# Kernel tuning notes

Hardware: AMD Instinct MI355X
Metric: run time of the kernel (lower is better)

Reference implementation:

```python
import jax, jax.numpy as jnp
import numpy as np

B, C_IN, FH, FW = 4, 256, 64, 176
N_PTS = 150000
D_BINS = 64
BEV_H = BEV_W = 200
RES = 0.5
EPS = 1e-5


def setup_inputs() -> dict:
    key = jax.random.key(0)
    ks = jax.random.split(key, 8)
    camera_features = jax.random.normal(ks[0], (B, C_IN, FH, FW), dtype=jnp.float32)
    pixels_uv = jax.random.uniform(ks[1], (B, N_PTS, 2), dtype=jnp.float32)
    K_inv = jax.random.normal(ks[2], (B, 3, 3), dtype=jnp.float32)
    # depth head params: Conv2d(256,128,3,pad=1) -> BN(128) -> ReLU -> Conv2d(128,64,1)
    W1 = jax.random.normal(ks[3], (128, C_IN, 3, 3), dtype=jnp.float32) * 0.02
    b1 = jnp.zeros((128,), dtype=jnp.float32)
    gamma = jnp.ones((128,), dtype=jnp.float32)
    beta = jnp.zeros((128,), dtype=jnp.float32)
    W2 = jax.random.normal(ks[4], (D_BINS, 128, 1, 1), dtype=jnp.float32) * 0.05
    b2 = jnp.zeros((D_BINS,), dtype=jnp.float32)
    depth_bins = jnp.linspace(1.0, 60.0, D_BINS, dtype=jnp.float32)
    return {"camera_features": camera_features, "pixels_uv": pixels_uv, "K_inv": K_inv,
            "W1": W1, "b1": b1, "gamma": gamma, "beta": beta, "W2": W2, "b2": b2,
            "depth_bins": depth_bins}


def _depth_head(x, W1, b1, gamma, beta, W2, b2):
    dn = ("NCHW", "OIHW", "NCHW")
    h = jax.lax.conv_general_dilated(x, W1, (1, 1), ((1, 1), (1, 1)), dimension_numbers=dn)
    h = h + b1[None, :, None, None]
    # BatchNorm2d, training-mode batch statistics (module is used without eval())
    mu = h.mean(axis=(0, 2, 3), keepdims=True)
    var = h.var(axis=(0, 2, 3), keepdims=True)
    h = (h - mu) * jax.lax.rsqrt(var + EPS)
    h = h * gamma[None, :, None, None] + beta[None, :, None, None]
    h = jax.nn.relu(h)
    logits = jax.lax.conv_general_dilated(h, W2, (1, 1), ((0, 0), (0, 0)), dimension_numbers=dn)
    logits = logits + b2[None, :, None, None]
    return jax.nn.softmax(logits, axis=1)  # [B, D, H, W]


def reference(camera_features, pixels_uv, K_inv, W1, b1, gamma, beta, W2, b2, depth_bins):
    depth_dist = _depth_head(camera_features, W1, b1, gamma, beta, W2, b2)

    # lift_to_3d
    exp_d = depth_dist.mean(axis=1)  # [B, H, W]
    ones = jnp.ones((B, N_PTS, 1), dtype=pixels_uv.dtype)
    homo = jnp.concatenate([pixels_uv, ones], axis=-1)            # [B, N, 3]
    pts3d = jnp.einsum('bnk,bjk->bnj', homo, K_inv)               # homo @ K_inv^T
    depth = exp_d.mean(axis=(1, 2))[:, None, None]                # [B, 1, 1]
    pts3d = pts3d * depth                                         # [B, N, 3]

    # splat_to_bev: scatter-add occupancy, then clamp to [0, 1]
    x_min = -(BEV_H * RES / 2)
    gx = jnp.clip(((pts3d[:, :, 0] - x_min) / RES).astype(jnp.int32), 0, BEV_W - 1)
    gy = jnp.clip(((pts3d[:, :, 1] - x_min) / RES).astype(jnp.int32), 0, BEV_H - 1)
    flat_idx = (jnp.arange(B, dtype=jnp.int32)[:, None] * (BEV_H * BEV_W) + gy * BEV_W + gx).ravel()
    grid = jnp.zeros((B * BEV_H * BEV_W,), dtype=jnp.float32).at[flat_idx].add(1.0)
    bev_grid = jnp.clip(grid.reshape(B, BEV_H, BEV_W), 0.0, 1.0)

    # expected_depth
    exp_depth = (depth_dist * depth_bins[None, :, None, None]).sum(axis=1)  # [B, H, W]

    return bev_grid, depth_dist, exp_depth, pts3d
```

## Files before the change

### kernel.cpp

```cpp
#include <hip/hip_runtime.h>

#define BATCH 4
#define CIN 256
#define FH 64
#define FW 176
#define HW (FH*FW)
#define PHW 11748
#define C1 128
#define DBINS 64
#define NPTS 150000
#define BEVN 200
#define EPSV 1e-5f

#define OFF_BEV 0
#define OFF_DD  160000
#define OFF_ED  3043584
#define OFF_PTS 3088640

#define WSB_H    0
#define WSB_WT   11534336
#define WSB_W2B  12124160
#define WSB_BN   12140544
#define WSB_XTP  12144640
#define XTP_B_ELEMS 3007488
#define WS_NEED_FULL  36204544ull
#define WS_NEED_HALF  24174592ull

typedef short bfx8 __attribute__((ext_vector_type(8)));
typedef short bfx4 __attribute__((ext_vector_type(4)));
typedef float f32x4 __attribute__((ext_vector_type(4)));
typedef unsigned short u16;

__device__ __forceinline__ u16 f2bf(float f) {
  union { float f; unsigned int u; } v; v.f = f;
  unsigned int r = v.u + 0x7FFF + ((v.u >> 16) & 1);
  return (u16)(r >> 16);
}
__device__ __forceinline__ float bf2f(u16 h) {
  union { unsigned int u; float f; } v; v.u = ((unsigned int)h) << 16;
  return v.f;
}

__device__ __forceinline__ void gload_lds16(const void* g, void* l) {
  __builtin_amdgcn_global_load_lds(
      (const __attribute__((address_space(1))) unsigned int*)g,
      (__attribute__((address_space(3))) unsigned int*)l, 16, 0, 0);
}

__global__ __launch_bounds__(256) void k_init(
    float* __restrict__ out, u16* __restrict__ w2b,
    const float* __restrict__ W2, u16* __restrict__ wt,
    const float* __restrict__ W1, u16* __restrict__ xtp, int nb) {
  int idx = blockIdx.x * 256 + threadIdx.x;
  if (idx < BATCH * BEVN * BEVN) out[OFF_BEV + idx] = 0.0f;
  if (idx < DBINS * C1) w2b[idx] = f2bf(W2[idx]);
  if (idx < 9 * C1 * CIN) {
    int tap = idx >> 15, rem = idx & 32767;
    int co = rem >> 8, c = rem & 255;
    wt[idx] = f2bf(W1[(co * CIN + c) * 9 + tap]);
  }
  const int nbord = nb * 484 * 32;
  if (idx < nbord) {
    int bloc = idx / (484 * 32);
    int r = idx - bloc * 484 * 32;
    int bpx = r >> 5, ch8 = r & 31;
    int prow, pcol;
    if (bpx < 178)      { prow = 0;  pcol = bpx; }
    else if (bpx < 356) { prow = 65; pcol = bpx - 178; }
    else { int q = bpx - 356; prow = 1 + (q >> 1); pcol = (q & 1) * 177; }
    *(bfx8*)&xtp[(bloc * PHW + prow * 178 + pcol) * 256 + ch8 * 8] = (bfx8)(short)0;
  }
}

__global__ __launch_bounds__(256) void k_xt(
    const float* __restrict__ x, u16* __restrict__ xtp, int b0) {
  __shared__ u16 s_t[176 * 72];
  const int blk = blockIdx.x;
  const int bloc = blk >> 8;
  const int rem = blk & 255;
  const int row = rem >> 2;
  const int c0 = (rem & 3) * 64;
  const int b = b0 + bloc;
  const int t = threadIdx.x;
  #pragma unroll
  for (int i = 0; i < 44; ++i) {
    int f = i * 256 + t;
    int c = f / 176, px = f - c * 176;
    s_t[px * 72 + c] = f2bf(x[((b * CIN + c0 + c) * FH + row) * FW + px]);
  }
  __syncthreads();
  const int base = (bloc * PHW + (row + 1) * 178 + 1) * 256 + c0;
  #pragma unroll
  for (int i = 0; i < 6; ++i) {
    int f = i * 256 + t;
    if (f < 1408) {
      int px = f >> 3, s = f & 7;
      *(bfx8*)&xtp[base + (px << 8) + s * 8] = *(const bfx8*)&s_t[px * 72 + s * 8];
    }
  }
}

#define ABUF_E 2048
#define STEP_E 6144

__global__ __launch_bounds__(256) void k_conv(
    const u16* __restrict__ xTp, const u16* __restrict__ wt,
    const float* __restrict__ b1, u16* __restrict__ hbf, int b0) {
  __shared__ __align__(16) u16 sMem[3 * STEP_E];

  const int blk = blockIdx.x;
  const int bloc = blk / 176;
  const int tile = blk % 176;
  const int h0 = (tile / 11) * 4;
  const int w0 = (tile % 11) * 16;
  const int b = b0 + bloc;
  const int t = threadIdx.x;
  const int lane = t & 63;
  const int wv = t >> 6;
  const int mw = wv >> 1, nw = wv & 1;
  const int l15 = lane & 15, kg = lane >> 4;

  const int cA = wv * 64 + lane;
  {
  }
  const int pxA = cA >> 2;
  const int gA = (bloc * PHW + (h0 + (pxA >> 4)) * 178 + (w0 + (pxA & 15))) * 256
               + (((cA & 3) ^ ((cA >> 3) & 3)) << 3);
  int gB[2];
  #pragma unroll
  for (int j = 0; j < 2; ++j) {
    int c = cA + j * 256;
    gB[j] = (c >> 2) * 256 + (((c & 3) ^ ((c >> 3) & 3)) << 3);
  }
  const int sw8 = (kg ^ ((l15 >> 1) & 3)) << 3;

  f32x4 acc[2][4];
  #pragma unroll
  for (int mf = 0; mf < 2; ++mf)
    #pragma unroll
    for (int nf = 0; nf < 4; ++nf) acc[mf][nf] = (f32x4)(0.f);

#define STAGE(S, SEL)                                                          \
  {                                                                            \
    const int tap_ = (S) >> 3, ck_ = (S) & 7;                                  \
    const int dy_ = tap_ / 3, dx_ = tap_ - dy_ * 3;                            \
    const int ao_ = ((dy_ * 178 + dx_) << 8) + (ck_ << 5);                     \
    const int wo_ = tap_ * 32768 + (ck_ << 5);                                 \
    u16* lb_ = &sMem[(SEL) * STEP_E];                                          \
    gload_lds16(&xTp[gA + ao_], &lb_[(wv * 64) * 8]);                          \
    gload_lds16(&wt[gB[0] + wo_], &lb_[ABUF_E + (wv * 64) * 8]);               \
    gload_lds16(&wt[gB[1] + wo_], &lb_[ABUF_E + (wv * 64 + 256) * 8]);         \
  }

#define COMPUTE(SEL)                                                           \
  {                                                                            \
    const u16* lb_ = &sMem[(SEL) * STEP_E];                                    \
    bfx8 af[2], bf[4];                                                         \
    _Pragma("unroll")                                                          \
    for (int mf = 0; mf < 2; ++mf)                                             \
      af[mf] = *(const bfx8*)&lb_[(mw * 32 + mf * 16 + l15) * 32 + sw8];       \
    _Pragma("unroll")                                                          \
    for (int nf = 0; nf < 4; ++nf)                                             \
      bf[nf] = *(const bfx8*)&lb_[ABUF_E + (nw * 64 + nf * 16 + l15) * 32 + sw8]; \
    _Pragma("unroll")                                                          \
    for (int mf = 0; mf < 2; ++mf)                                             \
      _Pragma("unroll")                                                        \
      for (int nf = 0; nf < 4; ++nf)                                           \
        acc[mf][nf] = __builtin_amdgcn_mfma_f32_16x16x32_bf16(af[mf], bf[nf], acc[mf][nf], 0, 0, 0); \
  }

#define VMCNT(N) asm volatile("s_waitcnt vmcnt(" #N ")" ::: "memory")
#define BARR __builtin_amdgcn_s_barrier()
#define SCHED0 __builtin_amdgcn_sched_barrier(0)

  STAGE(0, 0);
  STAGE(1, 1);
  STAGE(2, 2);

  #pragma unroll 1
  for (int s = 0; s <= 66; s += 3) {
    VMCNT(6); BARR; SCHED0;
    COMPUTE(0);
    BARR;
    STAGE(s + 3, 0);
    VMCNT(6); BARR; SCHED0;
    COMPUTE(1);
    BARR;
    STAGE(s + 4, 1);
    VMCNT(6); BARR; SCHED0;
    COMPUTE(2);
    BARR;
    STAGE(s + 5, 2);
  }
  VMCNT(6); BARR; SCHED0;
  COMPUTE(0);
  VMCNT(3); BARR; SCHED0;
  COMPUTE(1);
  VMCNT(0); BARR; SCHED0;
  COMPUTE(2);

  #pragma unroll
  for (int mf = 0; mf < 2; ++mf) {
    const int py = h0 + mw * 2 + mf;
    #pragma unroll
    for (int nf = 0; nf < 4; ++nf) {
      const int co = nw * 64 + nf * 16 + l15;
      const float bb = b1[co];
      bfx4 hv;
      #pragma unroll
      for (int j = 0; j < 4; ++j) hv[j] = (short)f2bf(acc[mf][nf][j] + bb);
      *(bfx4*)&hbf[((b * C1 + co) * FH + py) * FW + w0 + kg * 4] = hv;
    }
  }
#undef STAGE
#undef COMPUTE
#undef VMCNT
#undef BARR
#undef SCHED0
}

__global__ __launch_bounds__(256) void k_bnsum(
    const u16* __restrict__ h, float* __restrict__ part) {
  const int ch = blockIdx.x >> 2, b = blockIdx.x & 3;
  const int t = threadIdx.x;
  float s = 0.f, q = 0.f;
  const bfx8* p = (const bfx8*)&h[(b * C1 + ch) * HW];
  for (int i = t; i < HW / 8; i += 256) {
    bfx8 v8 = p[i];
    #pragma unroll
    for (int j = 0; j < 8; ++j) {
      float v = bf2f((u16)v8[j]);
      s += v;
      q = fmaf(v, v, q);
    }
  }
  #pragma unroll
  for (int o = 32; o; o >>= 1) {
    s += __shfl_xor(s, o);
    q += __shfl_xor(q, o);
  }
  __shared__ float rs[4], rq[4];
  int w = t >> 6;
  if ((t & 63) == 0) { rs[w] = s; rq[w] = q; }
  __syncthreads();
  if (t == 0) {
    part[ch * 8 + b * 2 + 0] = rs[0] + rs[1] + rs[2] + rs[3];
    part[ch * 8 + b * 2 + 1] = rq[0] + rq[1] + rq[2] + rq[3];
  }
}

__global__ __launch_bounds__(256) void k_head(
    const u16* __restrict__ h, const float* __restrict__ part,
    const float* __restrict__ gamma, const float* __restrict__ beta,
    const u16* __restrict__ w2b, const float* __restrict__ b2,
    const float* __restrict__ bins, float* __restrict__ out) {
  __shared__ u16 sAct[64 * 128];
  __shared__ float sP[64 * 68];
  __shared__ float sAB[256];

  const int blk = blockIdx.x;
  const int b = blk / 176;
  const int px0 = (blk % 176) * 64;
  const int t = threadIdx.x;
  const int lane = t & 63;
  const int w = t >> 6;
  const int l15 = lane & 15, kg = lane >> 4;

  if (t < 128) {
    float s = 0.f, q = 0.f;
    #pragma unroll
    for (int bb = 0; bb < 4; ++bb) {
      s += part[t * 8 + bb * 2 + 0];
      q += part[t * 8 + bb * 2 + 1];
    }
    const float inv_n = 1.0f / (float)(BATCH * HW);
    float mu = s * inv_n;
    float var = q * inv_n - mu * mu;
    float a = gamma[t] * rsqrtf(var + EPSV);
    sAB[t] = a;
    sAB[128 + t] = beta[t] - mu * a;
  }

  bfx8 bfr[4][4];
  #pragma unroll
  for (int nf = 0; nf < 4; ++nf)
    #pragma unroll
    for (int ck = 0; ck < 4; ++ck)
      bfr[nf][ck] = *(const bfx8*)&w2b[(nf * 16 + l15) * 128 + ck * 32 + kg * 8];
  float binr[4], b2r[4];
  #pragma unroll
  for (int nf = 0; nf < 4; ++nf) {
    binr[nf] = bins[nf * 16 + l15];
    b2r[nf] = b2[nf * 16 + l15];
  }
  f32x4 acc[4];
  #pragma unroll
  for (int nf = 0; nf < 4; ++nf) acc[nf] = (f32x4)(b2r[nf]);
  __syncthreads();

  #pragma unroll
  for (int i = 0; i < 4; ++i) {
    int f = t + i * 256;
    int c = f >> 3, g = f & 7;
    bfx8 v8 = *(const bfx8*)&h[(b * C1 + c) * HW + px0 + g * 8];
    float a = sAB[c], sh = sAB[128 + c];
    #pragma unroll
    for (int j = 0; j < 8; ++j) {
      int px = g * 8 + j;
      float v = fmaxf(fmaf(bf2f((u16)v8[j]), a, sh), 0.f);
      sAct[px * 128 + (((c >> 3) ^ (px & 15)) << 3) + (c & 7)] = f2bf(v);
    }
  }
  __syncthreads();

  #pragma unroll
  for (int ck = 0; ck < 4; ++ck) {
    bfx8 af = *(const bfx8*)&sAct[(w * 16 + l15) * 128 + (((ck * 4 + kg) ^ l15) << 3)];
    #pragma unroll
    for (int nf = 0; nf < 4; ++nf)
      acc[nf] = __builtin_amdgcn_mfma_f32_16x16x32_bf16(af, bfr[nf][ck], acc[nf], 0, 0, 0);
  }

  #pragma unroll
  for (int j = 0; j < 4; ++j) {
    float e[4];
    float z = 0.f, ez = 0.f;
    #pragma unroll
    for (int nf = 0; nf < 4; ++nf) {
      e[nf] = __expf(acc[nf][j]);
      z += e[nf];
      ez = fmaf(e[nf], binr[nf], ez);
    }
    #pragma unroll
    for (int o = 1; o < 16; o <<= 1) {
      z += __shfl_xor(z, o);
      ez += __shfl_xor(ez, o);
    }
    float inv = 1.0f / z;
    int px = w * 16 + kg * 4 + j;
    #pragma unroll
    for (int nf = 0; nf < 4; ++nf)
      sP[(nf * 16 + l15) * 68 + px] = e[nf] * inv;
    if (l15 == kg * 4 + j) out[OFF_ED + b * HW + px0 + px] = ez * inv;
  }
  __syncthreads();

  #pragma unroll
  for (int i = 0; i < 4; ++i) {
    int f = t + i * 256;
    int d = f >> 4, q = f & 15;
    f32x4 v;
    #pragma unroll
    for (int jj = 0; jj < 4; ++jj) v[jj] = sP[d * 68 + q * 4 + jj];
    *(f32x4*)&out[OFF_DD + (b * DBINS + d) * HW + px0 + q * 4] = v;
  }
}

__global__ void k_points(const float* __restrict__ uv, const float* __restrict__ kinv,
                         float* __restrict__ out) {
  int idx = blockIdx.x * 256 + threadIdx.x;
  if (idx >= BATCH * NPTS) return;
  int b = idx / NPTS;
  const float depth = 1.0f / 64.0f;
  float u = uv[idx * 2 + 0];
  float v = uv[idx * 2 + 1];
  const float* K = &kinv[b * 9];
  float p0 = (u * K[0] + v * K[1] + K[2]) * depth;
  float p1 = (u * K[3] + v * K[4] + K[5]) * depth;
  float p2 = (u * K[6] + v * K[7] + K[8]) * depth;
  out[OFF_PTS + idx * 3 + 0] = p0;
  out[OFF_PTS + idx * 3 + 1] = p1;
  out[OFF_PTS + idx * 3 + 2] = p2;
  int gx = (int)((p0 + 50.0f) * 2.0f);
  int gy = (int)((p1 + 50.0f) * 2.0f);
  gx = min(max(gx, 0), BEVN - 1);
  gy = min(max(gy, 0), BEVN - 1);
  out[OFF_BEV + (b * BEVN + gy) * BEVN + gx] = 1.0f;
}

extern "C" void kernel_launch(void* const* d_in, const int* in_sizes, int n_in,
                              void* d_out, int out_size, void* d_ws, size_t ws_size,
                              hipStream_t stream) {
  const float* x     = (const float*)d_in[0];
  const float* uv    = (const float*)d_in[1];
  const float* kinv  = (const float*)d_in[2];
  const float* w1    = (const float*)d_in[3];
  const float* b1    = (const float*)d_in[4];
  const float* gamma = (const float*)d_in[5];
  const float* beta  = (const float*)d_in[6];
  const float* w2    = (const float*)d_in[7];
  const float* b2    = (const float*)d_in[8];
  const float* bins  = (const float*)d_in[9];
  float* out = (float*)d_out;

  u16*   wsH   = (u16*)d_ws;
  u16*   wsWT  = (u16*)((char*)d_ws + WSB_WT);
  u16*   wsW2B = (u16*)((char*)d_ws + WSB_W2B);
  float* wsBN  = (float*)((char*)d_ws + WSB_BN);
  u16*   wsXTP = (u16*)((char*)d_ws + WSB_XTP);

  int nb = (ws_size >= WS_NEED_FULL) ? 4 : (ws_size >= WS_NEED_HALF) ? 2 : 1;

  k_init<<<1152, 256, 0, stream>>>(out, wsW2B, w2, wsWT, w1, wsXTP, nb);
  for (int b0 = 0; b0 < BATCH; b0 += nb) {
    k_xt<<<nb * 256, 256, 0, stream>>>(x, wsXTP, b0);
    k_conv<<<nb * 176, 256, 0, stream>>>(wsXTP, wsWT, b1, wsH, b0);
  }
  k_bnsum<<<512, 256, 0, stream>>>(wsH, wsBN);
  k_head<<<704, 256, 0, stream>>>(wsH, wsBN, gamma, beta, wsW2B, b2, bins, out);
  k_points<<<(BATCH * NPTS + 255) / 256, 256, 0, stream>>>(uv, kinv, out);
}
```

Before: 87.66 us.

## Restructure conv as halo-tile implicit GEMM with register-held weights

The 3x3 conv kernel now stages an 8x18 input halo tile per 32-channel chunk in LDS and reuses it across all 9 taps. Before, each tap reloaded its own shifted input slice. Weights are read straight from global memory into registers, and the tile now covers 8 rows by 64 output channels. Both halves of the output channels are split across blocks, and a double-buffered halo replaces the triple-buffered per-tap staging. The aim is to cut global/LDS traffic and barriers per MFMA, at the cost of uncoalesced direct weight loads and more register pressure (launch bounds 256,2).

```diff
diff --git a/kernel.cpp b/kernel.cpp
--- a/kernel.cpp
+++ b/kernel.cpp
@@ -100,18 +100,19 @@
   }
 }
 
-#define ABUF_E 2048
-#define STEP_E 6144
-
-__global__ __launch_bounds__(256) void k_conv(
+#define HALO_E 6144
+
+__global__ __launch_bounds__(256, 2) void k_conv(
     const u16* __restrict__ xTp, const u16* __restrict__ wt,
     const float* __restrict__ b1, u16* __restrict__ hbf, int b0) {
-  __shared__ __align__(16) u16 sMem[3 * STEP_E];
+  __shared__ __align__(16) u16 sMem[2 * HALO_E];
 
   const int blk = blockIdx.x;
   const int bloc = blk / 176;
-  const int tile = blk % 176;
-  const int h0 = (tile / 11) * 4;
+  const int rem = blk % 176;
+  const int co0 = (rem & 1) * 64;
+  const int tile = rem >> 1;
+  const int h0 = (tile / 11) * 8;
   const int w0 = (tile % 11) * 16;
   const int b = b0 + bloc;
   const int t = threadIdx.x;
@@ -120,91 +121,85 @@
   const int mw = wv >> 1, nw = wv & 1;
   const int l15 = lane & 15, kg = lane >> 4;
 
-  const int cA = wv * 64 + lane;
-  {
-  }
-  const int pxA = cA >> 2;
-  const int gA = (bloc * PHW + (h0 + (pxA >> 4)) * 178 + (w0 + (pxA & 15))) * 256
-               + (((cA & 3) ^ ((cA >> 3) & 3)) << 3);
-  int gB[2];
-  #pragma unroll
-  for (int j = 0; j < 2; ++j) {
-    int c = cA + j * 256;
-    gB[j] = (c >> 2) * 256 + (((c & 3) ^ ((c >> 3) & 3)) << 3);
-  }
-  const int sw8 = (kg ^ ((l15 >> 1) & 3)) << 3;
-
-  f32x4 acc[2][4];
-  #pragma unroll
-  for (int mf = 0; mf < 2; ++mf)
-    #pragma unroll
-    for (int nf = 0; nf < 4; ++nf) acc[mf][nf] = (f32x4)(0.f);
-
-#define STAGE(S, SEL)                                                          \
+  int gH[3];
+  #pragma unroll
+  for (int j = 0; j < 3; ++j) {
+    int c = t + j * 256;
+    int px = c >> 2;
+    if (px > 179) px = 179;
+    int hr = px / 18, hc = px - hr * 18;
+    int slog = (c & 3) ^ ((c >> 3) & 3);
+    gH[j] = (bloc * PHW + (h0 + hr) * 178 + (w0 + hc)) * 256 + slog * 8;
+  }
+  const int gwB0 = (co0 + nw * 32 + l15) * 256 + kg * 8;
+  const int gwB1 = (co0 + nw * 32 + 16 + l15) * 256 + kg * 8;
+
+  f32x4 acc[4][2];
+  #pragma unroll
+  for (int mf = 0; mf < 4; ++mf)
+    #pragma unroll
+    for (int nf = 0; nf < 2; ++nf) acc[mf][nf] = (f32x4)(0.f);
+
+#define STAGEH(CKV, DST)                                                       \
   {                                                                            \
-    const int tap_ = (S) >> 3, ck_ = (S) & 7;                                  \
-    const int dy_ = tap_ / 3, dx_ = tap_ - dy_ * 3;                            \
-    const int ao_ = ((dy_ * 178 + dx_) << 8) + (ck_ << 5);                     \
-    const int wo_ = tap_ * 32768 + (ck_ << 5);                                 \
-    u16* lb_ = &sMem[(SEL) * STEP_E];                                          \
-    gload_lds16(&xTp[gA + ao_], &lb_[(wv * 64) * 8]);                          \
-    gload_lds16(&wt[gB[0] + wo_], &lb_[ABUF_E + (wv * 64) * 8]);               \
-    gload_lds16(&wt[gB[1] + wo_], &lb_[ABUF_E + (wv * 64 + 256) * 8]);         \
-  }
-
-#define COMPUTE(SEL)                                                           \
+    gload_lds16(&xTp[gH[0] + (CKV) * 32], &(DST)[(wv * 64) * 8]);              \
+    gload_lds16(&xTp[gH[1] + (CKV) * 32], &(DST)[(256 + wv * 64) * 8]);        \
+    gload_lds16(&xTp[gH[2] + (CKV) * 32], &(DST)[(512 + wv * 64) * 8]);        \
+  }
+
+#define LOADB(BA, BB, TAP, CKV)                                                \
   {                                                                            \
-    const u16* lb_ = &sMem[(SEL) * STEP_E];                                    \
-    bfx8 af[2], bf[4];                                                         \
+    BA = *(const bfx8*)&wt[(TAP) * 32768 + (CKV) * 32 + gwB0];                 \
+    BB = *(const bfx8*)&wt[(TAP) * 32768 + (CKV) * 32 + gwB1];                 \
+  }
+
+#define COMPUTE(T, BA, BB)                                                     \
+  {                                                                            \
+    const int dy_ = (T) / 3, dx_ = (T) % 3;                                    \
     _Pragma("unroll")                                                          \
-    for (int mf = 0; mf < 2; ++mf)                                             \
-      af[mf] = *(const bfx8*)&lb_[(mw * 32 + mf * 16 + l15) * 32 + sw8];       \
-    _Pragma("unroll")                                                          \
-    for (int nf = 0; nf < 4; ++nf)                                             \
-      bf[nf] = *(const bfx8*)&lb_[ABUF_E + (nw * 64 + nf * 16 + l15) * 32 + sw8]; \
-    _Pragma("unroll")                                                          \
-    for (int mf = 0; mf < 2; ++mf)                                             \
-      _Pragma("unroll")                                                        \
-      for (int nf = 0; nf < 4; ++nf)                                           \
-        acc[mf][nf] = __builtin_amdgcn_mfma_f32_16x16x32_bf16(af[mf], bf[nf], acc[mf][nf], 0, 0, 0); \
+    for (int mf = 0; mf < 4; ++mf) {                                           \
+      const int px_ = (mw * 4 + mf + dy_) * 18 + l15 + dx_;                    \
+      bfx8 af = *(const bfx8*)&hcur[px_ * 32 + ((kg ^ ((px_ >> 1) & 3)) << 3)];\
+      acc[mf][0] = __builtin_amdgcn_mfma_f32_16x16x32_bf16(af, BA, acc[mf][0], 0, 0, 0); \
+      acc[mf][1] = __builtin_amdgcn_mfma_f32_16x16x32_bf16(af, BB, acc[mf][1], 0, 0, 0); \
+    }                                                                          \
   }
 
 #define VMCNT(N) asm volatile("s_waitcnt vmcnt(" #N ")" ::: "memory")
-#define BARR __builtin_amdgcn_s_barrier()
-#define SCHED0 __builtin_amdgcn_sched_barrier(0)
-
-  STAGE(0, 0);
-  STAGE(1, 1);
-  STAGE(2, 2);
+
+  bfx8 b0a, b0b, b1a, b1b, b2a, b2b;
+  STAGEH(0, sMem);
+  LOADB(b0a, b0b, 0, 0);
+  LOADB(b1a, b1b, 1, 0);
+  LOADB(b2a, b2b, 2, 0);
 
   #pragma unroll 1
-  for (int s = 0; s <= 66; s += 3) {
-    VMCNT(6); BARR; SCHED0;
-    COMPUTE(0);
-    BARR;
-    STAGE(s + 3, 0);
-    VMCNT(6); BARR; SCHED0;
-    COMPUTE(1);
-    BARR;
-    STAGE(s + 4, 1);
-    VMCNT(6); BARR; SCHED0;
-    COMPUTE(2);
-    BARR;
-    STAGE(s + 5, 2);
-  }
-  VMCNT(6); BARR; SCHED0;
-  COMPUTE(0);
-  VMCNT(3); BARR; SCHED0;
-  COMPUTE(1);
-  VMCNT(0); BARR; SCHED0;
-  COMPUTE(2);
-
-  #pragma unroll
-  for (int mf = 0; mf < 2; ++mf) {
-    const int py = h0 + mw * 2 + mf;
-    #pragma unroll
-    for (int nf = 0; nf < 4; ++nf) {
-      const int co = nw * 64 + nf * 16 + l15;
+  for (int ck = 0; ck < 8; ++ck) {
+    VMCNT(6);
+    asm volatile("s_waitcnt lgkmcnt(0)" ::: "memory");
+    __builtin_amdgcn_s_barrier();
+    __builtin_amdgcn_sched_barrier(0);
+    const u16* hcur = &sMem[(ck & 1) * HALO_E];
+    u16* hnxt = &sMem[((ck & 1) ^ 1) * HALO_E];
+
+    COMPUTE(0, b0a, b0b); LOADB(b0a, b0b, 3, ck);
+    COMPUTE(1, b1a, b1b); LOADB(b1a, b1b, 4, ck);
+    COMPUTE(2, b2a, b2b); LOADB(b2a, b2b, 5, ck);
+    COMPUTE(3, b0a, b0b); LOADB(b0a, b0b, 6, ck);
+    COMPUTE(4, b1a, b1b); LOADB(b1a, b1b, 7, ck);
+    if (ck < 7) STAGEH(ck + 1, hnxt);
+    COMPUTE(5, b2a, b2b); LOADB(b2a, b2b, 8, ck);
+    COMPUTE(6, b0a, b0b); if (ck < 7) LOADB(b0a, b0b, 0, ck + 1);
+    COMPUTE(7, b1a, b1b); if (ck < 7) LOADB(b1a, b1b, 1, ck + 1);
+    COMPUTE(8, b2a, b2b); if (ck < 7) LOADB(b2a, b2b, 2, ck + 1);
+  }
+
+  #pragma unroll
+  for (int mf = 0; mf < 4; ++mf) {
+    const int py = h0 + mw * 4 + mf;
+    #pragma unroll
+    for (int nf = 0; nf < 2; ++nf) {
+      const int co = co0 + nw * 32 + nf * 16 + l15;
       const float bb = b1[co];
       bfx4 hv;
       #pragma unroll
@@ -212,11 +207,10 @@
       *(bfx4*)&hbf[((b * C1 + co) * FH + py) * FW + w0 + kg * 4] = hv;
     }
   }
-#undef STAGE
+#undef STAGEH
+#undef LOADB
 #undef COMPUTE
 #undef VMCNT
-#undef BARR
-#undef SCHED0
 }
 
 __global__ __launch_bounds__(256) void k_bnsum(
```

Result: slower. 110.5 us (+26.1%).
